# Kernel optimization log

Hardware: AMD Instinct MI355X
Metric: run time of the kernel (lower is better)

The kernel has to match this reference:

```python
import jax, jax.numpy as jnp
import numpy as np
import math

B, N, ND, ED, CD, H = 4, 128, 256, 128, 256, 8
D = ND // H

def _ln(x):
    m = jnp.mean(x, axis=-1, keepdims=True)
    v = jnp.mean((x - m) ** 2, axis=-1, keepdims=True)
    return (x - m) / jnp.sqrt(v + 1e-5)

def _lrelu(x):
    return jax.nn.leaky_relu(x, negative_slope=0.1)

def setup_inputs() -> dict:
    key = jax.random.key(0)
    ks = jax.random.split(key, 16)
    rn = lambda k, s: jax.random.normal(k, s, jnp.float32) * 0.02
    return {
        "nodes": jax.random.normal(ks[0], (B, N, ND), jnp.float32),
        "edges": jax.random.normal(ks[1], (B, N, N, ED), jnp.float32),
        "conds": jax.random.normal(ks[2], (B, 1, CD), jnp.float32),
        "Wc": rn(ks[3], (CD, 4 * ND)), "bc": jnp.zeros((4 * ND,), jnp.float32),
        "Wqkv": rn(ks[4], (ND, 3 * ND)), "bqkv": jnp.zeros((3 * ND,), jnp.float32),
        "Wss": rn(ks[5], (ED, 2 * ND)), "bss": jnp.zeros((2 * ND,), jnp.float32),
        "Wno": rn(ks[6], (ND, ND)), "bno": jnp.zeros((ND,), jnp.float32),
        "Weo": rn(ks[7], (ND, ED)), "beo": jnp.zeros((ED,), jnp.float32),
        "Wn1": rn(ks[8], (ND, 4 * ND)), "bn1": jnp.zeros((4 * ND,), jnp.float32),
        "Wn2": rn(ks[9], (4 * ND, ND)), "bn2": jnp.zeros((ND,), jnp.float32),
        "We1": rn(ks[10], (ED, ED)), "be1": jnp.zeros((ED,), jnp.float32),
        "We2": rn(ks[11], (ED, ED)), "be2": jnp.zeros((ED,), jnp.float32),
    }

def reference(nodes, edges, conds, Wc, bc, Wqkv, bqkv, Wss, bss, Wno, bno, Weo, beo, Wn1, bn1, Wn2, bn2, We1, be1, We2, be2):
    b, n, _ = nodes.shape
    # FiLM conditioning (4 chunks, torch chunk order)
    cond = conds @ Wc + bc  # (b,1,4*ND)
    mul_in, add_in, mul_out, add_out = jnp.split(cond, 4, axis=-1)
    n_in = _lrelu(_ln(nodes) * (1.0 + mul_in) + add_in)
    e_in = _lrelu(_ln(edges))
    # attention
    qkv = n_in @ Wqkv + bqkv
    q, k, v = jnp.split(qkv, 3, axis=-1)
    q = q.reshape(b, n, H, D).transpose(0, 2, 1, 3)  # (b,h,n,d)
    k = k.reshape(b, n, H, D).transpose(0, 2, 1, 3)
    v = v.reshape(b, n, H, D).transpose(0, 2, 1, 3)
    # outer-product attention tensor (b,h,q,k,d)
    attn5 = q[:, :, :, None, :] * k[:, :, None, :, :]
    ss = e_in @ Wss + bss  # (b,n,n,2*ND)
    shift, scale = jnp.split(ss, 2, axis=-1)
    shift = shift.reshape(b, n, n, H, D).transpose(0, 3, 1, 2, 4)
    scale = scale.reshape(b, n, n, H, D).transpose(0, 3, 1, 2, 4)
    new_e = attn5 * scale + attn5 + shift  # (b,h,q,k,d)
    logits = jnp.sum(new_e, axis=4) / math.sqrt(D)  # (b,h,q,k)
    attn = jax.nn.softmax(logits, axis=2)  # softmax over dim=2 as in source
    # weighted values -> (b,n,H*D), matching values.view/transpose/flatten layout
    wv = jnp.einsum('bhqk,bhkd->bqhd', attn, v).reshape(b, n, ND)
    new_edges = new_e.transpose(0, 2, 3, 1, 4).reshape(b, n, n, ND)
    delta_nodes = wv @ Wno + bno
    delta_edges = _lrelu(new_edges) @ Weo + beo
    nodes = nodes + delta_nodes
    edges = edges + delta_edges
    # FiLM-normed MLP blocks
    n_out = _lrelu(_ln(nodes) * (1.0 + mul_out) + add_out)
    nodes = nodes + (_lrelu(n_out @ Wn1 + bn1) @ Wn2 + bn2)
    e_out = _lrelu(_ln(edges))
    edges = edges + (_lrelu(e_out @ We1 + be1) @ We2 + be2)
    return (nodes, edges)
```

## Files before the change

kernel.cpp:

```cpp
#include <hip/hip_runtime.h>
#include <hip/hip_bf16.h>

#define BB 4
#define NN 128
#define NH 8

typedef __attribute__((ext_vector_type(8))) short short8;
typedef __attribute__((ext_vector_type(4))) float f32x4;

__device__ __forceinline__ float lrelu(float x){ return fmaxf(x, 0.1f*x); }
__device__ __forceinline__ unsigned short f2b(float x){
  __hip_bfloat16 h = __float2bfloat16(x);
  return *reinterpret_cast<unsigned short*>(&h);
}
__device__ __forceinline__ short8 ldf(const unsigned short* p){ return *(const short8*)p; }


__global__ __launch_bounds__(256) void k_setup(
    const float* Wss, const float* Weo, const float* We1, const float* We2,
    const float* Wqkv, const float* Wno, const float* Wn1, const float* Wn2,
    const float* conds, const float* Wc, const float* bc,
    unsigned short* wbf, float* cond){
  __shared__ float tile[32][33];
  __shared__ float c[256];
  int bid = blockIdx.x, t = threadIdx.x;
  if (bid < 896){
    const float* src; int K, N; size_t doff; int tid;
    if      (bid < 64)  { src=Wss;  K=128;  N=512;  doff=0;      tid=bid; }
    else if (bid < 96)  { src=Weo;  K=256;  N=128;  doff=65536;  tid=bid-64; }
    else if (bid < 112) { src=We1;  K=128;  N=128;  doff=98304;  tid=bid-96; }
    else if (bid < 128) { src=We2;  K=128;  N=128;  doff=114688; tid=bid-112; }
    else if (bid < 320) { src=Wqkv; K=256;  N=768;  doff=131072; tid=bid-128; }
    else if (bid < 384) { src=Wno;  K=256;  N=256;  doff=327680; tid=bid-320; }
    else if (bid < 640) { src=Wn1;  K=256;  N=1024; doff=393216; tid=bid-384; }
    else                { src=Wn2;  K=1024; N=256;  doff=655360; tid=bid-640; }
    int ntk = K >> 5;
    int k0 = (tid % ntk) * 32, n0 = (tid / ntk) * 32;
    int r = t >> 3, c4 = (t & 7) * 4;
    float4 v = *(const float4*)(src + (size_t)(k0+r)*N + n0 + c4);
    tile[r][c4+0]=v.x; tile[r][c4+1]=v.y; tile[r][c4+2]=v.z; tile[r][c4+3]=v.w;
    __syncthreads();
    ushort4 o;
    o.x = f2b(tile[c4+0][r]); o.y = f2b(tile[c4+1][r]);
    o.z = f2b(tile[c4+2][r]); o.w = f2b(tile[c4+3][r]);
    *(ushort4*)(wbf + doff + (size_t)(n0+r)*K + k0 + c4) = o;
  } else {
    int i = bid - 896;
    int b = i >> 2, j = (i&3)*256 + t;
    c[t] = conds[(size_t)b*256 + t];
    __syncthreads();
    float acc = bc[j];
    for (int kk = 0; kk < 256; kk++) acc += c[kk]*Wc[(size_t)kk*1024 + j];
    cond[b*1024 + j] = acc;
  }
}

#define NSTR 260
__global__ __launch_bounds__(256) void k_nodeA(const float* __restrict__ nodes,
    const float* __restrict__ cond, const unsigned short* __restrict__ WqkvT,
    const float* __restrict__ bqkv, float* __restrict__ qbuf,
    float* __restrict__ kT, unsigned short* __restrict__ vT){
  __shared__ float nbuf[16*NSTR];
  __shared__ __align__(16) unsigned short abuf[16*272];
  __shared__ float psum[256], psq[256], mrow[16], irow[16];
  int t = threadIdx.x;
  int rg = blockIdx.x >> 2, slice = blockIdx.x & 3;
  int b = rg >> 3, n0 = (rg & 7)*16;
  int l = t & 63, w = t >> 6, l15 = l & 15, q = l >> 4;

  const float4* src = (const float4*)(nodes + ((size_t)(b*128+n0))*256);
  #pragma unroll
  for (int i = 0; i < 4; i++){
    int f = t + i*256; int r = f >> 6, c4 = f & 63;
    *(float4*)(nbuf + r*NSTR + c4*4) = src[f];
  }
  __syncthreads();
  {
    int r = t >> 4, p = t & 15;
    float s = 0.f, s2 = 0.f;
    #pragma unroll
    for (int i = 0; i < 16; i++){ float v = nbuf[r*NSTR + p + 16*i]; s += v; s2 += v*v; }
    psum[t] = s; psq[t] = s2;
  }
  __syncthreads();
  if (t < 16){
    float s = 0.f, s2 = 0.f;
    #pragma unroll
    for (int i = 0; i < 16; i++){ s += psum[t*16+i]; s2 += psq[t*16+i]; }
    float m = s*(1.f/256);
    mrow[t] = m; irow[t] = rsqrtf(s2*(1.f/256) - m*m + 1e-5f);
  }
  __syncthreads();
  #pragma unroll
  for (int i = 0; i < 16; i++){
    int f = t + i*256; int r = f >> 8, cc = f & 255;
    float x = (nbuf[r*NSTR+cc]-mrow[r])*irow[r]*(1.f+cond[b*1024+cc]) + cond[b*1024+256+cc];
    abuf[r*272+cc] = f2b(lrelu(x));
  }
  __syncthreads();
  short8 af[8];
  #pragma unroll
  for (int k = 0; k < 8; k++) af[k] = ldf(abuf + l15*272 + k*32 + q*8);
  #pragma unroll
  for (int tt = 0; tt < 3; tt++){
    int cc = slice*192 + w*48 + tt*16 + l15;
    const unsigned short* bp = WqkvT + (size_t)cc*256 + q*8;
    f32x4 acc = {0.f,0.f,0.f,0.f};
    #pragma unroll
    for (int k = 0; k < 8; k++) acc = __builtin_amdgcn_mfma_f32_16x16x32_bf16(af[k], ldf(bp + k*32), acc,0,0,0);
    float bb = bqkv[cc];
    if (cc < 256){
      #pragma unroll
      for (int r = 0; r < 4; r++) qbuf[(size_t)(b*128+n0+q*4+r)*256 + cc] = acc[r] + bb;
    } else if (cc < 512){
      float4 kv; kv.x = acc[0]+bb; kv.y = acc[1]+bb; kv.z = acc[2]+bb; kv.w = acc[3]+bb;
      *(float4*)(kT + ((size_t)(b*256 + cc-256))*128 + n0 + q*4) = kv;
    } else {
      ushort4 vv; vv.x = f2b(acc[0]+bb); vv.y = f2b(acc[1]+bb); vv.z = f2b(acc[2]+bb); vv.w = f2b(acc[3]+bb);
      *(ushort4*)(vT + ((size_t)(b*256 + cc-512))*128 + n0 + q*4) = vv;
    }
  }
}

#define ASTR 144
#define LSTR 264
__global__ __launch_bounds__(256) void k_edge(
    const float* __restrict__ edges, const float* __restrict__ qbuf, const float* __restrict__ kT,
    const unsigned short* __restrict__ WssT, const float* __restrict__ bss,
    const unsigned short* __restrict__ WeoT, const float* __restrict__ beo,
    const unsigned short* __restrict__ We1T, const float* __restrict__ be1,
    const unsigned short* __restrict__ We2T, const float* __restrict__ be2,
    float* __restrict__ logitsT, float* __restrict__ out_edges){
  __shared__ __align__(16) unsigned short abuf[64*ASTR];
  __shared__ __align__(16) unsigned short lbuf[64*LSTR];
  __shared__ float qvs[256];
  __shared__ float redS[64][4], redQ[64][4], mrow[64], irow[64];

  int t = threadIdx.x;
  int p0 = blockIdx.x * 64;
  int b  = p0 >> 14, qi = (p0 >> 7) & 127, ki0 = p0 & 127;
  int w = t >> 6, l15 = t & 15, q = (t & 63) >> 4;

  {
    qvs[t] = qbuf[(size_t)(b*128 + qi)*256 + t];
    const float4* src = (const float4*)(edges + (size_t)p0*128);
    #pragma unroll
    for (int i=0;i<8;i++){
      int idx = t + i*256;
      float4 ev = src[idx];
      int r = idx >> 5, c4 = idx & 31;
      float s  = ev.x + ev.y + ev.z + ev.w;
      float s2 = ev.x*ev.x + ev.y*ev.y + ev.z*ev.z + ev.w*ev.w;
      #pragma unroll
      for (int mm=1; mm<32; mm<<=1){ s += __shfl_xor(s,mm); s2 += __shfl_xor(s2,mm); }
      float m = s*(1.f/128);
      float inv = rsqrtf(s2*(1.f/128) - m*m + 1e-5f);
      ushort4 pk;
      pk.x = f2b(lrelu((ev.x - m)*inv)); pk.y = f2b(lrelu((ev.y - m)*inv));
      pk.z = f2b(lrelu((ev.z - m)*inv)); pk.w = f2b(lrelu((ev.w - m)*inv));
      *(ushort4*)(abuf + r*ASTR + c4*4) = pk;
    }
  }
  __syncthreads();

  const float isd = 0.17677669529663687f;
  {
    short8 af[4][4];
    #pragma unroll
    for (int s=0;s<4;s++)
      #pragma unroll
      for (int k=0;k<4;k++) af[s][k] = ldf(abuf + (s*16+l15)*ASTR + k*32 + q*8);
    #pragma unroll
    for (int h2=0; h2<2; h2++){
      int h = w*2 + h2;
      float ps[4][4] = {{0,0,0,0},{0,0,0,0},{0,0,0,0},{0,0,0,0}};
      #pragma unroll
      for (int tt=0; tt<2; tt++){
        int cc = h*32 + tt*16 + l15;
        const unsigned short* bsp = WssT + (size_t)cc*128 + q*8;
        const unsigned short* bcp = WssT + (size_t)(cc+256)*128 + q*8;
        f32x4 aS[4], aC[4];
        #pragma unroll
        for (int s=0;s<4;s++){ aS[s]={0.f,0.f,0.f,0.f}; aC[s]={0.f,0.f,0.f,0.f}; }
        #pragma unroll
        for (int k=0;k<4;k++){
          short8 b0 = ldf(bsp + k*32);
          short8 b1 = ldf(bcp + k*32);
          #pragma unroll
          for (int s=0;s<4;s++){
            aS[s] = __builtin_amdgcn_mfma_f32_16x16x32_bf16(af[s][k], b0, aS[s],0,0,0);
            aC[s] = __builtin_amdgcn_mfma_f32_16x16x32_bf16(af[s][k], b1, aC[s],0,0,0);
          }
        }
        float bS = bss[cc], bC = bss[256+cc], qv = qvs[cc];
        #pragma unroll
        for (int s=0;s<4;s++){
          float4 kv4 = *(const float4*)(kT + ((size_t)(b*256+cc))*128 + ki0 + s*16 + q*4);
          float kvv[4] = {kv4.x, kv4.y, kv4.z, kv4.w};
          #pragma unroll
          for (int r=0;r<4;r++){
            int row = s*16 + q*4 + r;
            float ne = qv*kvv[r]*(1.f + aC[s][r] + bC) + aS[s][r] + bS;
            lbuf[row*LSTR + cc] = f2b(lrelu(ne));
            ps[s][r] += ne;
          }
        }
      }
      #pragma unroll
      for (int s=0;s<4;s++)
        #pragma unroll
        for (int r=0;r<4;r++){
          float v = ps[s][r];
          v += __shfl_xor(v,1); v += __shfl_xor(v,2);
          v += __shfl_xor(v,4); v += __shfl_xor(v,8);
          if (l15 == 0){
            int ki = ki0 + s*16 + q*4 + r;
            logitsT[((size_t)(b*8+h)*128 + ki)*128 + qi] = v * isd;
          }
        }
    }
  }
  __syncthreads();

  float res[2][4][4];
  {
    f32x4 acc[2][4];
    #pragma unroll
    for (int tt=0;tt<2;tt++)
      #pragma unroll
      for (int s=0;s<4;s++) acc[tt][s] = {0.f,0.f,0.f,0.f};
    #pragma unroll
    for (int k=0;k<8;k++){
      short8 lf[4];
      #pragma unroll
      for (int s=0;s<4;s++) lf[s] = ldf(lbuf + (s*16+l15)*LSTR + k*32 + q*8);
      #pragma unroll
      for (int tt=0;tt<2;tt++){
        int ec = w*32 + tt*16 + l15;
        short8 bf = ldf(WeoT + (size_t)ec*256 + k*32 + q*8);
        #pragma unroll
        for (int s=0;s<4;s++)
          acc[tt][s] = __builtin_amdgcn_mfma_f32_16x16x32_bf16(lf[s], bf, acc[tt][s],0,0,0);
      }
    }
    #pragma unroll
    for (int tt=0;tt<2;tt++){
      int ec = w*32 + tt*16 + l15;
      float bb = beo[ec];
      #pragma unroll
      for (int s=0;s<4;s++)
        #pragma unroll
        for (int r=0;r<4;r++){
          int row = s*16 + q*4 + r;
          res[tt][s][r] = edges[(size_t)(p0+row)*128 + ec] + acc[tt][s][r] + bb;
        }
    }
  }
  #pragma unroll
  for (int s=0;s<4;s++)
    #pragma unroll
    for (int r=0;r<4;r++){
      float ps = res[0][s][r] + res[1][s][r];
      float p2 = res[0][s][r]*res[0][s][r] + res[1][s][r]*res[1][s][r];
      ps += __shfl_xor(ps,1); ps += __shfl_xor(ps,2); ps += __shfl_xor(ps,4); ps += __shfl_xor(ps,8);
      p2 += __shfl_xor(p2,1); p2 += __shfl_xor(p2,2); p2 += __shfl_xor(p2,4); p2 += __shfl_xor(p2,8);
      if (l15 == 0){ redS[s*16+q*4+r][w] = ps; redQ[s*16+q*4+r][w] = p2; }
    }
  __syncthreads();
  if (t < 64){
    float s = redS[t][0]+redS[t][1]+redS[t][2]+redS[t][3];
    float s2 = redQ[t][0]+redQ[t][1]+redQ[t][2]+redQ[t][3];
    float m = s*(1.f/128);
    mrow[t] = m; irow[t] = rsqrtf(s2*(1.f/128) - m*m + 1e-5f);
  }
  __syncthreads();
  #pragma unroll
  for (int tt=0;tt<2;tt++){
    int ec = w*32 + tt*16 + l15;
    #pragma unroll
    for (int s=0;s<4;s++)
      #pragma unroll
      for (int r=0;r<4;r++){
        int row = s*16 + q*4 + r;
        abuf[row*ASTR + ec] = f2b(lrelu((res[tt][s][r] - mrow[row])*irow[row]));
      }
  }
  __syncthreads();

  unsigned short* hbuf = lbuf;
  {
    f32x4 acc[2][4];
    #pragma unroll
    for (int tt=0;tt<2;tt++)
      #pragma unroll
      for (int s=0;s<4;s++) acc[tt][s] = {0.f,0.f,0.f,0.f};
    #pragma unroll
    for (int k=0;k<4;k++){
      short8 af2[4];
      #pragma unroll
      for (int s=0;s<4;s++) af2[s] = ldf(abuf + (s*16+l15)*ASTR + k*32 + q*8);
      #pragma unroll
      for (int tt=0;tt<2;tt++){
        int ec = w*32 + tt*16 + l15;
        short8 bf = ldf(We1T + (size_t)ec*128 + k*32 + q*8);
        #pragma unroll
        for (int s=0;s<4;s++)
          acc[tt][s] = __builtin_amdgcn_mfma_f32_16x16x32_bf16(af2[s], bf, acc[tt][s],0,0,0);
      }
    }
    #pragma unroll
    for (int tt=0;tt<2;tt++){
      int ec = w*32 + tt*16 + l15;
      float bb = be1[ec];
      #pragma unroll
      for (int s=0;s<4;s++)
        #pragma unroll
        for (int r=0;r<4;r++)
          hbuf[(s*16+q*4+r)*ASTR + ec] = f2b(lrelu(acc[tt][s][r] + bb));
    }
  }
  __syncthreads();
  {
    f32x4 acc[2][4];
    #pragma unroll
    for (int tt=0;tt<2;tt++)
      #pragma unroll
      for (int s=0;s<4;s++) acc[tt][s] = {0.f,0.f,0.f,0.f};
    #pragma unroll
    for (int k=0;k<4;k++){
      short8 hf[4];
      #pragma unroll
      for (int s=0;s<4;s++) hf[s] = ldf(hbuf + (s*16+l15)*ASTR + k*32 + q*8);
      #pragma unroll
      for (int tt=0;tt<2;tt++){
        int ec = w*32 + tt*16 + l15;
        short8 bf = ldf(We2T + (size_t)ec*128 + k*32 + q*8);
        #pragma unroll
        for (int s=0;s<4;s++)
          acc[tt][s] = __builtin_amdgcn_mfma_f32_16x16x32_bf16(hf[s], bf, acc[tt][s],0,0,0);
      }
    }
    #pragma unroll
    for (int tt=0;tt<2;tt++){
      int ec = w*32 + tt*16 + l15;
      float bb = be2[ec];
      #pragma unroll
      for (int s=0;s<4;s++)
        #pragma unroll
        for (int r=0;r<4;r++){
          int row = s*16 + q*4 + r;
          out_edges[(size_t)(p0+row)*128 + ec] = res[tt][s][r] + acc[tt][s][r] + bb;
        }
    }
  }
}

__global__ __launch_bounds__(256) void k_attn(const float* __restrict__ logitsT,
                                              unsigned short* __restrict__ attnB){
  __shared__ float tile[16][132];
  __shared__ float mS[16], sS[16];
  int bh = blockIdx.x >> 3, slice = blockIdx.x & 7;
  int t = threadIdx.x, w = t >> 6, l = t & 63;
  const float* base = logitsT + (size_t)bh*16384 + slice*16*128;
  #pragma unroll
  for (int i = 0; i < 8; i++){
    int idx = t + i*256; int ki = idx >> 7, qq = idx & 127;
    tile[ki][qq] = base[ki*128 + qq];
  }
  __syncthreads();
  #pragma unroll
  for (int i = 0; i < 4; i++){
    int ki = w*4 + i;
    float x0 = tile[ki][l], x1 = tile[ki][l+64];
    float mx = fmaxf(x0, x1);
    #pragma unroll
    for (int m=1;m<64;m<<=1) mx = fmaxf(mx, __shfl_xor(mx,m));
    float s = __expf(x0-mx) + __expf(x1-mx);
    #pragma unroll
    for (int m=1;m<64;m<<=1) s += __shfl_xor(s,m);
    if (l == 0){ mS[ki] = mx; sS[ki] = 1.f/s; }
  }
  __syncthreads();
  unsigned short* obase = attnB + (size_t)bh*16384 + slice*16;
  #pragma unroll
  for (int i = 0; i < 8; i++){
    int idx = t + i*256; int qq = idx >> 4, kk = idx & 15;
    obase[qq*128 + kk] = f2b(__expf(tile[kk][qq] - mS[kk]) * sS[kk]);
  }
}

#define AB 272
__global__ __launch_bounds__(256) void k_nodeB(
    const unsigned short* __restrict__ attnB, const unsigned short* __restrict__ vT,
    const float* __restrict__ nodes, const float* __restrict__ cond,
    const unsigned short* __restrict__ WnoT, const float* __restrict__ bno,
    const unsigned short* __restrict__ Wn1T, const float* __restrict__ bn1,
    float* __restrict__ nodes1ws, unsigned short* __restrict__ hiddenB){
  __shared__ __align__(16) unsigned short abuf[16*AB];
  __shared__ float redS[16][4], redQ[16][4], mrow[16], irow[16];
  int t = threadIdx.x;
  int rg = blockIdx.x >> 2, slice = blockIdx.x & 3;
  int b = rg >> 3, n0 = (rg & 7)*16;
  int w = t >> 6, l15 = t & 15, q = (t & 63) >> 4;

  #pragma unroll
  for (int h2=0; h2<2; h2++){
    int h = w*2 + h2;
    const unsigned short* ap = attnB + ((size_t)(b*8+h)*128 + n0 + l15)*128 + q*8;
    short8 af[4];
    #pragma unroll
    for (int k=0;k<4;k++) af[k] = ldf(ap + k*32);
    #pragma unroll
    for (int tt=0;tt<2;tt++){
      int cc = h*32 + tt*16 + l15;
      const unsigned short* bp = vT + (size_t)(b*256+cc)*128 + q*8;
      f32x4 acc = {0.f,0.f,0.f,0.f};
      #pragma unroll
      for (int k=0;k<4;k++) acc = __builtin_amdgcn_mfma_f32_16x16x32_bf16(af[k], ldf(bp + k*32), acc,0,0,0);
      #pragma unroll
      for (int r=0;r<4;r++) abuf[(q*4+r)*AB + cc] = f2b(acc[r]);
    }
  }
  __syncthreads();

  float res[4][4];
  {
    short8 aw[8];
    #pragma unroll
    for (int k=0;k<8;k++) aw[k] = ldf(abuf + l15*AB + k*32 + q*8);
    #pragma unroll
    for (int tt=0;tt<4;tt++){
      int cc = w*64 + tt*16 + l15;
      const unsigned short* bp = WnoT + (size_t)cc*256 + q*8;
      f32x4 acc = {0.f,0.f,0.f,0.f};
      #pragma unroll
      for (int k=0;k<8;k++) acc = __builtin_amdgcn_mfma_f32_16x16x32_bf16(aw[k], ldf(bp + k*32), acc,0,0,0);
      float bb = bno[cc];
      #pragma unroll
      for (int r=0;r<4;r++)
        res[tt][r] = nodes[(size_t)(b*128+n0+q*4+r)*256 + cc] + acc[r] + bb;
    }
  }
  #pragma unroll
  for (int r=0;r<4;r++){
    float ps = res[0][r]+res[1][r]+res[2][r]+res[3][r];
    float p2 = res[0][r]*res[0][r]+res[1][r]*res[1][r]+res[2][r]*res[2][r]+res[3][r]*res[3][r];
    ps += __shfl_xor(ps,1); ps += __shfl_xor(ps,2); ps += __shfl_xor(ps,4); ps += __shfl_xor(ps,8);
    p2 += __shfl_xor(p2,1); p2 += __shfl_xor(p2,2); p2 += __shfl_xor(p2,4); p2 += __shfl_xor(p2,8);
    if (l15 == 0){ redS[q*4+r][w] = ps; redQ[q*4+r][w] = p2; }
  }
  __syncthreads();
  if (t < 16){
    float s = redS[t][0]+redS[t][1]+redS[t][2]+redS[t][3];
    float s2 = redQ[t][0]+redQ[t][1]+redQ[t][2]+redQ[t][3];
    float m = s*(1.f/256);
    mrow[t] = m; irow[t] = rsqrtf(s2*(1.f/256) - m*m + 1e-5f);
  }
  __syncthreads();
  #pragma unroll
  for (int tt=0;tt<4;tt++){
    int cc = w*64 + tt*16 + l15;
    float mul = 1.f + cond[b*1024 + 512 + cc];
    float add = cond[b*1024 + 768 + cc];
    #pragma unroll
    for (int r=0;r<4;r++){
      int row = q*4+r;
      abuf[row*AB + cc] = f2b(lrelu((res[tt][r] - mrow[row])*irow[row]*mul + add));
    }
  }
  if (slice == 0){
    #pragma unroll
    for (int tt=0;tt<4;tt++){
      int cc = w*64 + tt*16 + l15;
      #pragma unroll
      for (int r=0;r<4;r++)
        nodes1ws[(size_t)(rg*16 + q*4+r)*256 + cc] = res[tt][r];
    }
  }
  __syncthreads();
  {
    short8 a2[8];
    #pragma unroll
    for (int k=0;k<8;k++) a2[k] = ldf(abuf + l15*AB + k*32 + q*8);
    #pragma unroll
    for (int tt=0;tt<4;tt++){
      int cc = slice*256 + w*64 + tt*16 + l15;
      const unsigned short* bp = Wn1T + (size_t)cc*256 + q*8;
      f32x4 acc = {0.f,0.f,0.f,0.f};
      #pragma unroll
      for (int k=0;k<8;k++) acc = __builtin_amdgcn_mfma_f32_16x16x32_bf16(a2[k], ldf(bp + k*32), acc,0,0,0);
      float bb = bn1[cc];
      #pragma unroll
      for (int r=0;r<4;r++)
        hiddenB[((size_t)rg*16 + q*4+r)*1024 + cc] = f2b(lrelu(acc[r] + bb));
    }
  }
}

__global__ __launch_bounds__(256) void k_nodeC(
    const unsigned short* __restrict__ hiddenB, const float* __restrict__ nodes1ws,
    const unsigned short* __restrict__ Wn2T, const float* __restrict__ bn2,
    float* __restrict__ out_nodes){
  int t = threadIdx.x;
  int rg = blockIdx.x >> 2, cs = blockIdx.x & 3;
  int w = t >> 6, l15 = t & 15, q = (t & 63) >> 4;
  int cc = cs*64 + w*16 + l15;
  const unsigned short* ap = hiddenB + ((size_t)rg*16 + l15)*1024 + q*8;
  const unsigned short* bp = Wn2T + (size_t)cc*1024 + q*8;
  f32x4 acc = {0.f,0.f,0.f,0.f};
  #pragma unroll
  for (int k=0;k<32;k++)
    acc = __builtin_amdgcn_mfma_f32_16x16x32_bf16(ldf(ap + k*32), ldf(bp + k*32), acc,0,0,0);
  float bb = bn2[cc];
  #pragma unroll
  for (int r=0;r<4;r++){
    size_t row = (size_t)rg*16 + q*4 + r;
    out_nodes[row*256 + cc] = nodes1ws[row*256 + cc] + acc[r] + bb;
  }
}

extern "C" void kernel_launch(void* const* d_in, const int* in_sizes, int n_inp,
                              void* d_out, int out_size, void* d_ws, size_t ws_size,
                              hipStream_t stream){
  const float* nodes = (const float*)d_in[0];
  const float* edges = (const float*)d_in[1];
  const float* conds = (const float*)d_in[2];
  const float* Wc   = (const float*)d_in[3];
  const float* bc   = (const float*)d_in[4];
  const float* Wqkv = (const float*)d_in[5];
  const float* bqkv = (const float*)d_in[6];
  const float* Wss  = (const float*)d_in[7];
  const float* bss  = (const float*)d_in[8];
  const float* Wno  = (const float*)d_in[9];
  const float* bno  = (const float*)d_in[10];
  const float* Weo  = (const float*)d_in[11];
  const float* beo  = (const float*)d_in[12];
  const float* Wn1  = (const float*)d_in[13];
  const float* bn1  = (const float*)d_in[14];
  const float* Wn2  = (const float*)d_in[15];
  const float* bn2  = (const float*)d_in[16];
  const float* We1  = (const float*)d_in[17];
  const float* be1  = (const float*)d_in[18];
  const float* We2  = (const float*)d_in[19];
  const float* be2  = (const float*)d_in[20];

  float* ws       = (float*)d_ws;
  float* cond     = ws;
  float* qbuf     = cond + 4096;
  float* kT       = qbuf + 131072;
  float* logitsT  = kT + 131072;
  float* nodes1ws = logitsT + 524288;
  unsigned short* attnB   = (unsigned short*)(nodes1ws + 131072);
  unsigned short* vT      = attnB + 524288;
  unsigned short* hiddenB = vT + 131072;
  unsigned short* wbf     = hiddenB + 524288;

  unsigned short* WssT  = wbf;
  unsigned short* WeoT  = wbf + 65536;
  unsigned short* We1T  = wbf + 98304;
  unsigned short* We2T  = wbf + 114688;
  unsigned short* WqkvT = wbf + 131072;
  unsigned short* WnoT  = wbf + 327680;
  unsigned short* Wn1T  = wbf + 393216;
  unsigned short* Wn2T  = wbf + 655360;

  float* out_nodes = (float*)d_out;
  float* out_edges = out_nodes + 131072;

  k_setup<<<912, 256, 0, stream>>>(Wss, Weo, We1, We2, Wqkv, Wno, Wn1, Wn2,
                                   conds, Wc, bc, wbf, cond);
  k_nodeA<<<128, 256, 0, stream>>>(nodes, cond, WqkvT, bqkv, qbuf, kT, vT);
  k_edge<<<BB*NN*NN/64, 256, 0, stream>>>(edges, qbuf, kT, WssT, bss, WeoT, beo,
                                          We1T, be1, We2T, be2, logitsT, out_edges);
  k_attn<<<BB*NH*8, 256, 0, stream>>>(logitsT, attnB);
  k_nodeB<<<128, 256, 0, stream>>>(attnB, vT, nodes, cond, WnoT, bno, Wn1T, bn1,
                                   nodes1ws, hiddenB);
  k_nodeC<<<128, 256, 0, stream>>>(hiddenB, nodes1ws, Wn2T, bn2, out_nodes);
}
```

Baseline: 218.7 us.

## Split softmax into stats kernel and fuse normalization into nodeB; alias k_edge shared memory

Logits are now stored q-major, and the softmax kernel that wrote a bf16 attention tensor is replaced by a small kernel that computes per-column max and reciprocal sum. k_nodeB applies exp and normalization while loading its MFMA operands. This removes one full write and read of the attention matrix, at the cost of a low-parallelism stats kernel (32 blocks, strided column reads) and extra exp work in nodeB. k_edge shared memory is consolidated by aliasing the reduction arrays onto lbuf with an added barrier, and ASTR is changed, which may raise occupancy. nodeC splits its MFMA chain into two accumulators for ILP.

```diff
diff --git a/kernel.cpp b/kernel.cpp
--- a/kernel.cpp
+++ b/kernel.cpp
@@ -122,7 +122,7 @@
   }
 }
 
-#define ASTR 144
+#define ASTR 136
 #define LSTR 264
 __global__ __launch_bounds__(256) void k_edge(
     const float* __restrict__ edges, const float* __restrict__ qbuf, const float* __restrict__ kT,
@@ -130,11 +130,15 @@
     const unsigned short* __restrict__ WeoT, const float* __restrict__ beo,
     const unsigned short* __restrict__ We1T, const float* __restrict__ be1,
     const unsigned short* __restrict__ We2T, const float* __restrict__ be2,
-    float* __restrict__ logitsT, float* __restrict__ out_edges){
-  __shared__ __align__(16) unsigned short abuf[64*ASTR];
-  __shared__ __align__(16) unsigned short lbuf[64*LSTR];
-  __shared__ float qvs[256];
-  __shared__ float redS[64][4], redQ[64][4], mrow[64], irow[64];
+    float* __restrict__ logits, float* __restrict__ out_edges){
+  __shared__ __align__(16) unsigned char SM[52224];
+  unsigned short* abuf = (unsigned short*)SM;
+  unsigned short* lbuf = (unsigned short*)(SM + 17408);
+  float* qvs = (float*)(SM + 51200);
+  float* redS = (float*)(SM + 17408);
+  float* redQ = (float*)(SM + 18432);
+  float* mrow = (float*)(SM + 19456);
+  float* irow = (float*)(SM + 19712);
 
   int t = threadIdx.x;
   int p0 = blockIdx.x * 64;
@@ -215,7 +219,7 @@
           v += __shfl_xor(v,4); v += __shfl_xor(v,8);
           if (l15 == 0){
             int ki = ki0 + s*16 + q*4 + r;
-            logitsT[((size_t)(b*8+h)*128 + ki)*128 + qi] = v * isd;
+            logits[((size_t)(b*8+h)*128 + qi)*128 + ki] = v * isd;
           }
         }
     }
@@ -256,6 +260,7 @@
         }
     }
   }
+  __syncthreads();
   #pragma unroll
   for (int s=0;s<4;s++)
     #pragma unroll
@@ -264,12 +269,12 @@
       float p2 = res[0][s][r]*res[0][s][r] + res[1][s][r]*res[1][s][r];
       ps += __shfl_xor(ps,1); ps += __shfl_xor(ps,2); ps += __shfl_xor(ps,4); ps += __shfl_xor(ps,8);
       p2 += __shfl_xor(p2,1); p2 += __shfl_xor(p2,2); p2 += __shfl_xor(p2,4); p2 += __shfl_xor(p2,8);
-      if (l15 == 0){ redS[s*16+q*4+r][w] = ps; redQ[s*16+q*4+r][w] = p2; }
+      if (l15 == 0){ redS[(s*16+q*4+r)*4 + w] = ps; redQ[(s*16+q*4+r)*4 + w] = p2; }
     }
   __syncthreads();
   if (t < 64){
-    float s = redS[t][0]+redS[t][1]+redS[t][2]+redS[t][3];
-    float s2 = redQ[t][0]+redQ[t][1]+redQ[t][2]+redQ[t][3];
+    float s = redS[t*4]+redS[t*4+1]+redS[t*4+2]+redS[t*4+3];
+    float s2 = redQ[t*4]+redQ[t*4+1]+redQ[t*4+2]+redQ[t*4+3];
     float m = s*(1.f/128);
     mrow[t] = m; irow[t] = rsqrtf(s2*(1.f/128) - m*m + 1e-5f);
   }
@@ -355,43 +360,25 @@
   }
 }
 
-__global__ __launch_bounds__(256) void k_attn(const float* __restrict__ logitsT,
-                                              unsigned short* __restrict__ attnB){
-  __shared__ float tile[16][132];
-  __shared__ float mS[16], sS[16];
-  int bh = blockIdx.x >> 3, slice = blockIdx.x & 7;
-  int t = threadIdx.x, w = t >> 6, l = t & 63;
-  const float* base = logitsT + (size_t)bh*16384 + slice*16*128;
-  #pragma unroll
-  for (int i = 0; i < 8; i++){
-    int idx = t + i*256; int ki = idx >> 7, qq = idx & 127;
-    tile[ki][qq] = base[ki*128 + qq];
-  }
-  __syncthreads();
-  #pragma unroll
-  for (int i = 0; i < 4; i++){
-    int ki = w*4 + i;
-    float x0 = tile[ki][l], x1 = tile[ki][l+64];
-    float mx = fmaxf(x0, x1);
-    #pragma unroll
-    for (int m=1;m<64;m<<=1) mx = fmaxf(mx, __shfl_xor(mx,m));
-    float s = __expf(x0-mx) + __expf(x1-mx);
-    #pragma unroll
-    for (int m=1;m<64;m<<=1) s += __shfl_xor(s,m);
-    if (l == 0){ mS[ki] = mx; sS[ki] = 1.f/s; }
-  }
-  __syncthreads();
-  unsigned short* obase = attnB + (size_t)bh*16384 + slice*16;
-  #pragma unroll
-  for (int i = 0; i < 8; i++){
-    int idx = t + i*256; int qq = idx >> 4, kk = idx & 15;
-    obase[qq*128 + kk] = f2b(__expf(tile[kk][qq] - mS[kk]) * sS[kk]);
-  }
+__global__ __launch_bounds__(128) void k_stats(const float* __restrict__ logits,
+                                               float* __restrict__ mstat,
+                                               float* __restrict__ sstat){
+  int bh = blockIdx.x, ki = threadIdx.x;
+  const float* base = logits + (size_t)bh*16384 + ki;
+  float mx = -3.4e38f;
+  #pragma unroll 8
+  for (int qi = 0; qi < 128; qi++) mx = fmaxf(mx, base[(size_t)qi*128]);
+  float s = 0.f;
+  #pragma unroll 8
+  for (int qi = 0; qi < 128; qi++) s += __expf(base[(size_t)qi*128] - mx);
+  mstat[bh*128 + ki] = mx;
+  sstat[bh*128 + ki] = 1.f/s;
 }
 
 #define AB 272
 __global__ __launch_bounds__(256) void k_nodeB(
-    const unsigned short* __restrict__ attnB, const unsigned short* __restrict__ vT,
+    const float* __restrict__ logits, const float* __restrict__ mstat, const float* __restrict__ sstat,
+    const unsigned short* __restrict__ vT,
     const float* __restrict__ nodes, const float* __restrict__ cond,
     const unsigned short* __restrict__ WnoT, const float* __restrict__ bno,
     const unsigned short* __restrict__ Wn1T, const float* __restrict__ bn1,
@@ -406,10 +393,30 @@
   #pragma unroll
   for (int h2=0; h2<2; h2++){
     int h = w*2 + h2;
-    const unsigned short* ap = attnB + ((size_t)(b*8+h)*128 + n0 + l15)*128 + q*8;
+    const float* lp = logits + ((size_t)(b*8+h)*128 + n0 + l15)*128;
+    const float* mp = mstat + (size_t)(b*8+h)*128;
+    const float* sp = sstat + (size_t)(b*8+h)*128;
     short8 af[4];
     #pragma unroll
-    for (int k=0;k<4;k++) af[k] = ldf(ap + k*32);
+    for (int k=0;k<4;k++){
+      int kb = q*8 + k*32;
+      float4 x0 = *(const float4*)(lp + kb);
+      float4 x1 = *(const float4*)(lp + kb + 4);
+      float4 m0 = *(const float4*)(mp + kb);
+      float4 m1 = *(const float4*)(mp + kb + 4);
+      float4 s0 = *(const float4*)(sp + kb);
+      float4 s1 = *(const float4*)(sp + kb + 4);
+      short8 v;
+      v[0] = (short)f2b(__expf(x0.x - m0.x)*s0.x);
+      v[1] = (short)f2b(__expf(x0.y - m0.y)*s0.y);
+      v[2] = (short)f2b(__expf(x0.z - m0.z)*s0.z);
+      v[3] = (short)f2b(__expf(x0.w - m0.w)*s0.w);
+      v[4] = (short)f2b(__expf(x1.x - m1.x)*s1.x);
+      v[5] = (short)f2b(__expf(x1.y - m1.y)*s1.y);
+      v[6] = (short)f2b(__expf(x1.z - m1.z)*s1.z);
+      v[7] = (short)f2b(__expf(x1.w - m1.w)*s1.w);
+      af[k] = v;
+    }
     #pragma unroll
     for (int tt=0;tt<2;tt++){
       int cc = h*32 + tt*16 + l15;
@@ -507,10 +514,13 @@
   int cc = cs*64 + w*16 + l15;
   const unsigned short* ap = hiddenB + ((size_t)rg*16 + l15)*1024 + q*8;
   const unsigned short* bp = Wn2T + (size_t)cc*1024 + q*8;
-  f32x4 acc = {0.f,0.f,0.f,0.f};
-  #pragma unroll
-  for (int k=0;k<32;k++)
-    acc = __builtin_amdgcn_mfma_f32_16x16x32_bf16(ldf(ap + k*32), ldf(bp + k*32), acc,0,0,0);
+  f32x4 acc0 = {0.f,0.f,0.f,0.f}, acc1 = acc0;
+  #pragma unroll
+  for (int k=0;k<16;k++){
+    acc0 = __builtin_amdgcn_mfma_f32_16x16x32_bf16(ldf(ap + k*32), ldf(bp + k*32), acc0,0,0,0);
+    acc1 = __builtin_amdgcn_mfma_f32_16x16x32_bf16(ldf(ap + (k+16)*32), ldf(bp + (k+16)*32), acc1,0,0,0);
+  }
+  f32x4 acc = acc0 + acc1;
   float bb = bn2[cc];
   #pragma unroll
   for (int r=0;r<4;r++){
@@ -548,10 +558,11 @@
   float* cond     = ws;
   float* qbuf     = cond + 4096;
   float* kT       = qbuf + 131072;
-  float* logitsT  = kT + 131072;
-  float* nodes1ws = logitsT + 524288;
-  unsigned short* attnB   = (unsigned short*)(nodes1ws + 131072);
-  unsigned short* vT      = attnB + 524288;
+  float* logits   = kT + 131072;
+  float* nodes1ws = logits + 524288;
+  float* mstat    = nodes1ws + 131072;
+  float* sstat    = mstat + 4096;
+  unsigned short* vT      = (unsigned short*)(sstat + 4096);
   unsigned short* hiddenB = vT + 131072;
   unsigned short* wbf     = hiddenB + 524288;
 
@@ -571,9 +582,9 @@
                                    conds, Wc, bc, wbf, cond);
   k_nodeA<<<128, 256, 0, stream>>>(nodes, cond, WqkvT, bqkv, qbuf, kT, vT);
   k_edge<<<BB*NN*NN/64, 256, 0, stream>>>(edges, qbuf, kT, WssT, bss, WeoT, beo,
-                                          We1T, be1, We2T, be2, logitsT, out_edges);
-  k_attn<<<BB*NH*8, 256, 0, stream>>>(logitsT, attnB);
-  k_nodeB<<<128, 256, 0, stream>>>(attnB, vT, nodes, cond, WnoT, bno, Wn1T, bn1,
-                                   nodes1ws, hiddenB);
+                                          We1T, be1, We2T, be2, logits, out_edges);
+  k_stats<<<BB*NH, 128, 0, stream>>>(logits, mstat, sstat);
+  k_nodeB<<<128, 256, 0, stream>>>(logits, mstat, sstat, vT, nodes, cond,
+                                   WnoT, bno, Wn1T, bn1, nodes1ws, hiddenB);
   k_nodeC<<<128, 256, 0, stream>>>(hiddenB, nodes1ws, Wn2T, bn2, out_nodes);
 }
```

Measured after the change: 239.5 us. +9.5%, slower.

## Widen node kernels' grids and split Wn2 GEMM over K with atomics

Applied to the files above, without the earlier changes.

Node-side kernels get more blocks: nodeA goes from 4 to 6 column slices per row group, nodeB from 4 to 8 hidden slices, and nodeC splits the 1024-long reduction into 4 K-chunks whose partial sums are combined with atomicAdd. nodeB now writes the residual plus bn2 straight into the output, so the nodes1ws workspace round trip is gone. The goal is better use of the GPU's compute units by the small node GEMMs, which previously ran only 128 blocks. The cost is atomic traffic, order-dependent float summation, and redundant prologue work (LayerNorm and attn@V) repeated in each extra block.

```diff
diff --git a/kernel.cpp b/kernel.cpp
--- a/kernel.cpp
+++ b/kernel.cpp
@@ -64,7 +64,7 @@
   __shared__ __align__(16) unsigned short abuf[16*272];
   __shared__ float psum[256], psq[256], mrow[16], irow[16];
   int t = threadIdx.x;
-  int rg = blockIdx.x >> 2, slice = blockIdx.x & 3;
+  int rg = blockIdx.x / 6, slice = blockIdx.x % 6;
   int b = rg >> 3, n0 = (rg & 7)*16;
   int l = t & 63, w = t >> 6, l15 = l & 15, q = l >> 4;
 
@@ -102,8 +102,8 @@
   #pragma unroll
   for (int k = 0; k < 8; k++) af[k] = ldf(abuf + l15*272 + k*32 + q*8);
   #pragma unroll
-  for (int tt = 0; tt < 3; tt++){
-    int cc = slice*192 + w*48 + tt*16 + l15;
+  for (int tt = 0; tt < 2; tt++){
+    int cc = slice*128 + w*32 + tt*16 + l15;
     const unsigned short* bp = WqkvT + (size_t)cc*256 + q*8;
     f32x4 acc = {0.f,0.f,0.f,0.f};
     #pragma unroll
@@ -395,11 +395,12 @@
     const float* __restrict__ nodes, const float* __restrict__ cond,
     const unsigned short* __restrict__ WnoT, const float* __restrict__ bno,
     const unsigned short* __restrict__ Wn1T, const float* __restrict__ bn1,
-    float* __restrict__ nodes1ws, unsigned short* __restrict__ hiddenB){
+    const float* __restrict__ bn2,
+    float* __restrict__ out_nodes, unsigned short* __restrict__ hiddenB){
   __shared__ __align__(16) unsigned short abuf[16*AB];
   __shared__ float redS[16][4], redQ[16][4], mrow[16], irow[16];
   int t = threadIdx.x;
-  int rg = blockIdx.x >> 2, slice = blockIdx.x & 3;
+  int rg = blockIdx.x >> 3, slice = blockIdx.x & 7;
   int b = rg >> 3, n0 = (rg & 7)*16;
   int w = t >> 6, l15 = t & 15, q = (t & 63) >> 4;
 
@@ -472,9 +473,10 @@
     #pragma unroll
     for (int tt=0;tt<4;tt++){
       int cc = w*64 + tt*16 + l15;
+      float bb = bn2[cc];
       #pragma unroll
       for (int r=0;r<4;r++)
-        nodes1ws[(size_t)(rg*16 + q*4+r)*256 + cc] = res[tt][r];
+        out_nodes[(size_t)(rg*16 + q*4+r)*256 + cc] = res[tt][r] + bb;
     }
   }
   __syncthreads();
@@ -483,8 +485,8 @@
     #pragma unroll
     for (int k=0;k<8;k++) a2[k] = ldf(abuf + l15*AB + k*32 + q*8);
     #pragma unroll
-    for (int tt=0;tt<4;tt++){
-      int cc = slice*256 + w*64 + tt*16 + l15;
+    for (int tt=0;tt<2;tt++){
+      int cc = slice*128 + w*32 + tt*16 + l15;
       const unsigned short* bp = Wn1T + (size_t)cc*256 + q*8;
       f32x4 acc = {0.f,0.f,0.f,0.f};
       #pragma unroll
@@ -498,24 +500,28 @@
 }
 
 __global__ __launch_bounds__(256) void k_nodeC(
-    const unsigned short* __restrict__ hiddenB, const float* __restrict__ nodes1ws,
-    const unsigned short* __restrict__ Wn2T, const float* __restrict__ bn2,
+    const unsigned short* __restrict__ hiddenB,
+    const unsigned short* __restrict__ Wn2T,
     float* __restrict__ out_nodes){
   int t = threadIdx.x;
-  int rg = blockIdx.x >> 2, cs = blockIdx.x & 3;
+  int rg = blockIdx.x >> 4;
+  int rem = blockIdx.x & 15;
+  int cs = rem >> 2, ks = rem & 3;
   int w = t >> 6, l15 = t & 15, q = (t & 63) >> 4;
   int cc = cs*64 + w*16 + l15;
-  const unsigned short* ap = hiddenB + ((size_t)rg*16 + l15)*1024 + q*8;
-  const unsigned short* bp = Wn2T + (size_t)cc*1024 + q*8;
-  f32x4 acc = {0.f,0.f,0.f,0.f};
-  #pragma unroll
-  for (int k=0;k<32;k++)
-    acc = __builtin_amdgcn_mfma_f32_16x16x32_bf16(ldf(ap + k*32), ldf(bp + k*32), acc,0,0,0);
-  float bb = bn2[cc];
+  const unsigned short* ap = hiddenB + ((size_t)rg*16 + l15)*1024 + ks*256 + q*8;
+  const unsigned short* bp = Wn2T + (size_t)cc*1024 + ks*256 + q*8;
+  f32x4 acc0 = {0.f,0.f,0.f,0.f}, acc1 = acc0;
+  #pragma unroll
+  for (int k=0;k<4;k++){
+    acc0 = __builtin_amdgcn_mfma_f32_16x16x32_bf16(ldf(ap + k*32), ldf(bp + k*32), acc0,0,0,0);
+    acc1 = __builtin_amdgcn_mfma_f32_16x16x32_bf16(ldf(ap + (k+4)*32), ldf(bp + (k+4)*32), acc1,0,0,0);
+  }
+  f32x4 acc = acc0 + acc1;
   #pragma unroll
   for (int r=0;r<4;r++){
     size_t row = (size_t)rg*16 + q*4 + r;
-    out_nodes[row*256 + cc] = nodes1ws[row*256 + cc] + acc[r] + bb;
+    atomicAdd(&out_nodes[row*256 + cc], acc[r]);
   }
 }
 
@@ -549,8 +555,7 @@
   float* qbuf     = cond + 4096;
   float* kT       = qbuf + 131072;
   float* logitsT  = kT + 131072;
-  float* nodes1ws = logitsT + 524288;
-  unsigned short* attnB   = (unsigned short*)(nodes1ws + 131072);
+  unsigned short* attnB   = (unsigned short*)(logitsT + 524288);
   unsigned short* vT      = attnB + 524288;
   unsigned short* hiddenB = vT + 131072;
   unsigned short* wbf     = hiddenB + 524288;
@@ -569,11 +574,11 @@
 
   k_setup<<<912, 256, 0, stream>>>(Wss, Weo, We1, We2, Wqkv, Wno, Wn1, Wn2,
                                    conds, Wc, bc, wbf, cond);
-  k_nodeA<<<128, 256, 0, stream>>>(nodes, cond, WqkvT, bqkv, qbuf, kT, vT);
+  k_nodeA<<<192, 256, 0, stream>>>(nodes, cond, WqkvT, bqkv, qbuf, kT, vT);
   k_edge<<<BB*NN*NN/64, 256, 0, stream>>>(edges, qbuf, kT, WssT, bss, WeoT, beo,
                                           We1T, be1, We2T, be2, logitsT, out_edges);
   k_attn<<<BB*NH*8, 256, 0, stream>>>(logitsT, attnB);
-  k_nodeB<<<128, 256, 0, stream>>>(attnB, vT, nodes, cond, WnoT, bno, Wn1T, bn1,
-                                   nodes1ws, hiddenB);
-  k_nodeC<<<128, 256, 0, stream>>>(hiddenB, nodes1ws, Wn2T, bn2, out_nodes);
-}
+  k_nodeB<<<256, 256, 0, stream>>>(attnB, vT, nodes, cond, WnoT, bno, Wn1T, bn1,
+                                   bn2, out_nodes, hiddenB);
+  k_nodeC<<<512, 256, 0, stream>>>(hiddenB, Wn2T, out_nodes);
+}
```

Result: no change. 214.8 us (-1.8%).
